# Kernel tuning notes

Hardware: AMD Instinct MI355X
Metric: run time of the kernel (lower is better)

Reference implementation:

```python
import jax, jax.numpy as jnp
import numpy as np

B, T, D, H, L, V = 8, 1024, 1024, 16, 4, 50257
HD = D // H
DF = 4 * D
EPS = 1e-5


def _layernorm(x, w, b):
    m = jnp.mean(x, axis=-1, keepdims=True)
    v = jnp.mean((x - m) ** 2, axis=-1, keepdims=True)
    return (x - m) * jax.lax.rsqrt(v + EPS) * w + b


def setup_inputs() -> dict:
    key = jax.random.key(0)
    ks = jax.random.split(key, 17)
    s = 0.02
    n = lambda k, shape: (jax.random.normal(k, shape) * s).astype(jnp.float32)
    return {
        "idx": jax.random.randint(ks[0], (B, T), 0, V),
        "tok_emb": n(ks[1], (V, D)),
        "pos_emb": n(ks[2], (T, D)),
        "wq": n(ks[3], (L, D, D)),
        "wk": n(ks[4], (L, D, D)),
        "wv": n(ks[5], (L, D, D)),
        "w_proj": n(ks[6], (L, D, D)),
        "b_proj": jnp.zeros((L, D), jnp.float32),
        "ln1_w": jnp.ones((L, D), jnp.float32),
        "ln1_b": jnp.zeros((L, D), jnp.float32),
        "ln2_w": jnp.ones((L, D), jnp.float32),
        "ln2_b": jnp.zeros((L, D), jnp.float32),
        "w1": n(ks[7], (L, D, DF)),
        "b1": jnp.zeros((L, DF), jnp.float32),
        "w2": n(ks[8], (L, DF, D)),
        "b2": jnp.zeros((L, D), jnp.float32),
    }


def reference(idx, tok_emb, pos_emb, wq, wk, wv, w_proj, b_proj,
              ln1_w, ln1_b, ln2_w, ln2_b, w1, b1, w2, b2):
    b, t = idx.shape
    x = tok_emb[idx] + pos_emb[:t]  # [B,T,D]
    causal_mask = jnp.tril(jnp.ones((t, t), dtype=bool))  # [T,T]
    # NOTE: original scales by full embedding dim C**-0.5, not head_size
    scale = jnp.asarray(D, x.dtype) ** -0.5
    for l in range(L):
        h = _layernorm(x, ln1_w[l], ln1_b[l])
        q = (h @ wq[l]).reshape(b, t, H, HD)
        k = (h @ wk[l]).reshape(b, t, H, HD)
        v = (h @ wv[l]).reshape(b, t, H, HD)
        scores = jnp.einsum('bthd,bshd->bhts', q, k) * scale  # [B,H,T,T]
        scores = jnp.where(causal_mask, scores, -jnp.inf)
        attn = jax.nn.softmax(scores, axis=-1)
        ctx = jnp.einsum('bhts,bshd->bthd', attn, v).reshape(b, t, D)
        x = x + (ctx @ w_proj[l] + b_proj[l])
        h2 = _layernorm(x, ln2_w[l], ln2_b[l])
        ff = jax.nn.relu(h2 @ w1[l] + b1[l]) @ w2[l] + b2[l]
        x = x + ff  # fRes = 1.0 (linear_residual=True)
    return x
```

## Files before the change

### kernel.cpp

```cpp
#include <hip/hip_runtime.h>
#include <hip/hip_bf16.h>
#include <stdint.h>

typedef __hip_bfloat16 bf16;
typedef __attribute__((ext_vector_type(8))) short short8;
typedef __attribute__((ext_vector_type(4))) float f32x4;
typedef __attribute__((ext_vector_type(2))) unsigned int uint32x2;

static constexpr int TB = 8;
static constexpr int TT = 1024;
static constexpr int TD = 1024;
static constexpr int TH = 16;
static constexpr int TL = 4;
static constexpr int TDF = 4096;
static constexpr int TM = TB * TT;
static constexpr int QS = 3072;

#if __has_builtin(__builtin_amdgcn_permlane16_swap) && __has_builtin(__builtin_amdgcn_permlane32_swap)
#define USE_PERMLANE 1
#else
#define USE_PERMLANE 0
#endif

#define GLOAD16(g, l) __builtin_amdgcn_global_load_lds( \
    (const __attribute__((address_space(1))) unsigned int*)(g), \
    (__attribute__((address_space(3))) unsigned int*)(l), 16, 0, 0)

__global__ __launch_bounds__(256) void k_embed(const int* __restrict__ idx,
        const float* __restrict__ tok, const float* __restrict__ pos,
        bf16* __restrict__ xbf) {
    int row = blockIdx.x;
    int t = row & (TT - 1);
    int token = idx[row];
    int c = threadIdx.x * 4;
    float4 tv = *(const float4*)(tok + (int64_t)token * TD + c);
    float4 pv = *(const float4*)(pos + (int64_t)t * TD + c);
    bf16 t4[4];
    t4[0] = __float2bfloat16(tv.x + pv.x);
    t4[1] = __float2bfloat16(tv.y + pv.y);
    t4[2] = __float2bfloat16(tv.z + pv.z);
    t4[3] = __float2bfloat16(tv.w + pv.w);
    *(uint2*)(xbf + (int64_t)row * TD + c) = *(uint2*)t4;
}

__global__ __launch_bounds__(256) void k_ln(const bf16* __restrict__ x,
        const float* __restrict__ w, const float* __restrict__ b,
        bf16* __restrict__ out) {
    int row = blockIdx.x;
    int tid = threadIdx.x;
    const bf16* xr = x + (int64_t)row * TD;
    uint2 raw = *(const uint2*)(xr + tid * 4);
    const bf16* rp = (const bf16*)&raw;
    float v0 = __bfloat162float(rp[0]), v1 = __bfloat162float(rp[1]);
    float v2 = __bfloat162float(rp[2]), v3 = __bfloat162float(rp[3]);
    float s  = v0 + v1 + v2 + v3;
    float s2 = v0*v0 + v1*v1 + v2*v2 + v3*v3;
    #pragma unroll
    for (int off = 32; off; off >>= 1) { s += __shfl_xor(s, off); s2 += __shfl_xor(s2, off); }
    __shared__ float red[8];
    int wv_ = tid >> 6, ln_ = tid & 63;
    if (ln_ == 0) { red[wv_] = s; red[4 + wv_] = s2; }
    __syncthreads();
    s  = red[0] + red[1] + red[2] + red[3];
    s2 = red[4] + red[5] + red[6] + red[7];
    float mean = s * (1.f / TD);
    float var  = s2 * (1.f / TD) - mean * mean;
    float rstd = rsqrtf(var + 1e-5f);
    float4 wv4 = *(const float4*)(w + tid * 4);
    float4 bv4 = *(const float4*)(b + tid * 4);
    bf16 t4[4];
    t4[0] = __float2bfloat16((v0 - mean) * rstd * wv4.x + bv4.x);
    t4[1] = __float2bfloat16((v1 - mean) * rstd * wv4.y + bv4.y);
    t4[2] = __float2bfloat16((v2 - mean) * rstd * wv4.z + bv4.z);
    t4[3] = __float2bfloat16((v3 - mean) * rstd * wv4.w + bv4.w);
    *(uint2*)(out + (int64_t)row * TD + tid * 4) = *(uint2*)t4;
}

__global__ __launch_bounds__(256) void k_wt(
        const float* __restrict__ wq, const float* __restrict__ wk,
        const float* __restrict__ wv, const float* __restrict__ wp,
        const float* __restrict__ w1, const float* __restrict__ w2,
        bf16* __restrict__ qkvT, bf16* __restrict__ wpT,
        bf16* __restrict__ w1T, bf16* __restrict__ w2T) {
    __shared__ bf16 tile[64 * 74];
    const int id = blockIdx.x;
    const float* src; bf16* dst; int K, N, n0, k0;
    if (id < 768) {
        int w = id >> 8, r = id & 255;
        src = (w == 0) ? wq : ((w == 1) ? wk : wv);
        dst = qkvT + (int64_t)w * 1024 * 1024;
        K = 1024; N = 1024; n0 = (r & 15) * 64; k0 = (r >> 4) * 64;
    } else if (id < 1024) {
        int r = id - 768; src = wp; dst = wpT;
        K = 1024; N = 1024; n0 = (r & 15) * 64; k0 = (r >> 4) * 64;
    } else if (id < 2048) {
        int r = id - 1024; src = w1; dst = w1T;
        K = 1024; N = 4096; n0 = (r & 63) * 64; k0 = (r >> 6) * 64;
    } else {
        int r = id - 2048; src = w2; dst = w2T;
        K = 4096; N = 1024; n0 = (r & 15) * 64; k0 = (r >> 4) * 64;
    }
    const int tid = threadIdx.x;
    #pragma unroll
    for (int i = 0; i < 16; i++) {
        int q = i * 256 + tid;
        int r = q >> 6, c = q & 63;
        tile[r * 74 + c] = __float2bfloat16(src[(int64_t)(k0 + r) * N + n0 + c]);
    }
    __syncthreads();
    #pragma unroll
    for (int i = 0; i < 16; i++) {
        int q = i * 256 + tid;
        int nr = q >> 6, kc = q & 63;
        dst[(int64_t)(n0 + nr) * K + k0 + kc] = tile[kc * 74 + nr];
    }
}

template<int EPI>
__global__ __launch_bounds__(512, 2) void k_gemm256(const bf16* __restrict__ A,
        const bf16* __restrict__ BT, const float* __restrict__ bias,
        float* __restrict__ outF, bf16* __restrict__ outB,
        bf16* __restrict__ vtp, int M, int N, int K) {
    extern __shared__ __align__(16) char smem[];
    const int tid = threadIdx.x;
    const int lane = tid & 63, wave = tid >> 6;
    const int wm = wave >> 2, wn = wave & 3;
    const int lr = lane & 15, lk = lane >> 4;
    const int nb = gridDim.x;
    const int sb = (blockIdx.x & 7) * (nb >> 3) + (blockIdx.x >> 3);
    const int nbn = N >> 8;
    const int bm = sb / nbn, bn = sb % nbn;
    const int64_t aBase = (int64_t)bm * 256 * K;
    const int64_t bBase = (int64_t)bn * 256 * K;
    const int NT = K >> 6;

    const int tswz = tid ^ (((tid >> 5) & 1) << 1);
    const int row0 = tswz >> 3, s0 = tswz & 7;

#define STAGE256(tt) do { \
        char* Ad_ = smem + (((tt) & 1) << 15); \
        char* Bd_ = smem + 65536 + (((tt) & 1) << 15); \
        _Pragma("unroll") \
        for (int j = 0; j < 4; j++) { \
            const int rr_ = j * 64 + row0; \
            GLOAD16(A  + aBase + (int64_t)rr_ * K + (tt) * 64 + s0 * 8, Ad_ + (j * 512 + tid) * 16); \
            GLOAD16(BT + bBase + (int64_t)rr_ * K + (tt) * 64 + s0 * 8, Bd_ + (j * 512 + tid) * 16); \
        } \
    } while (0)

    f32x4 acc[8][4] = {};
    const int lkx = lk ^ ((lr & 4) >> 1);
    const int aoff = wm * 8192 + lr * 64 + lkx * 8;
    const int boff = wn * 4096 + lr * 64 + lkx * 8;

    STAGE256(0);
    STAGE256(1);
    asm volatile("s_waitcnt vmcnt(8)" ::: "memory");
    __builtin_amdgcn_s_barrier();

    for (int t = 0; t < NT; ++t) {
        const bf16* Ab = (const bf16*)(smem + ((t & 1) << 15));
        const bf16* Bb = (const bf16*)(smem + 65536 + ((t & 1) << 15));
        short8 af[2][8], bv[2][4];
        #pragma unroll
        for (int kk = 0; kk < 2; kk++) {
            #pragma unroll
            for (int m = 0; m < 8; m++)
                af[kk][m] = *(const short8*)(Ab + aoff + m * 1024 + kk * 32);
            #pragma unroll
            for (int n = 0; n < 4; n++)
                bv[kk][n] = *(const short8*)(Bb + boff + n * 1024 + kk * 32);
        }
        asm volatile("s_waitcnt lgkmcnt(0)" ::: "memory");
        __builtin_amdgcn_sched_barrier(0);
        __builtin_amdgcn_s_barrier();
        if (t + 2 < NT) STAGE256(t + 2);
        __builtin_amdgcn_s_setprio(1);
        #pragma unroll
        for (int kk = 0; kk < 2; kk++)
            #pragma unroll
            for (int fm = 0; fm < 8; fm++)
                #pragma unroll
                for (int fn = 0; fn < 4; fn++)
                    acc[fm][fn] = __builtin_amdgcn_mfma_f32_16x16x32_bf16(
                        af[kk][fm], bv[kk][fn], acc[fm][fn], 0, 0, 0);
        __builtin_amdgcn_s_setprio(0);
        if (t + 2 < NT) {
            asm volatile("s_waitcnt vmcnt(8)" ::: "memory");
            __builtin_amdgcn_s_barrier();
        } else if (t + 1 < NT) {
            asm volatile("s_waitcnt vmcnt(0)" ::: "memory");
            __builtin_amdgcn_s_barrier();
        }
    }
#undef STAGE256

    #pragma unroll
    for (int fm = 0; fm < 8; fm++) {
        #pragma unroll
        for (int fn = 0; fn < 4; fn++) {
            const int col = bn * 256 + wn * 64 + fn * 16 + lr;
            if constexpr (EPI & 16) {
                const int trow = bm * 256 + wm * 128 + fm * 16 + lk * 4;
                if (col >= 2048) {
                    const int d = col - 2048;
                    bf16 t4[4];
                    #pragma unroll
                    for (int r = 0; r < 4; r++)
                        t4[r] = __float2bfloat16(acc[fm][fn][r]);
                    const int bb = trow >> 10, tt2 = trow & 1023;
                    *(uint2*)(vtp + ((int64_t)((bb * TH + (d >> 6)) * 64 + (d & 63)) * TT + tt2)) = *(uint2*)t4;
                } else {
                    #pragma unroll
                    for (int r = 0; r < 4; r++)
                        outB[(int64_t)(trow + r) * N + col] = __float2bfloat16(acc[fm][fn][r]);
                }
            } else {
                #pragma unroll
                for (int r = 0; r < 4; r++) {
                    const int row = bm * 256 + wm * 128 + fm * 16 + lk * 4 + r;
                    float v = acc[fm][fn][r];
                    if constexpr (EPI & 1) v += bias[col];
                    if constexpr (EPI & 2) v = fmaxf(v, 0.f);
                    if constexpr (EPI & 8) outF[(int64_t)row * N + col] = v;
                    else outB[(int64_t)row * N + col] = __float2bfloat16(v);
                }
            }
        }
    }
}

template<int EPI>
__global__ __launch_bounds__(512, 2) void k_gemm128d(const bf16* __restrict__ A,
        const bf16* __restrict__ BT, const float* __restrict__ bias,
        const bf16* __restrict__ residB,
        float* __restrict__ outF, bf16* __restrict__ outB, int M, int N, int K) {
    extern __shared__ __align__(16) char smem[];
    const int tid = threadIdx.x;
    const int lane = tid & 63, wave = tid >> 6;
    const int wm = wave >> 2, wn = wave & 3;
    const int lr = lane & 15, lk = lane >> 4;
    const int nb = gridDim.x;
    const int sb = (blockIdx.x & 7) * (nb >> 3) + (blockIdx.x >> 3);
    const int nbn = N >> 7;
    const int bm = sb / nbn, bn = sb % nbn;
    const int64_t aBase = (int64_t)bm * 128 * K;
    const int64_t bBase = (int64_t)bn * 128 * K;
    const int NT = K >> 6;

    const int tswz = tid ^ (((tid >> 5) & 1) << 1);
    const int row0 = tswz >> 3, s0 = tswz & 7;

#define STAGE128D(tt) do { \
        char* Ad_ = smem + (((tt) & 1) << 14); \
        char* Bd_ = smem + 32768 + (((tt) & 1) << 14); \
        _Pragma("unroll") \
        for (int j = 0; j < 2; j++) { \
            const int rr_ = j * 64 + row0; \
            GLOAD16(A  + aBase + (int64_t)rr_ * K + (tt) * 64 + s0 * 8, Ad_ + (j * 512 + tid) * 16); \
            GLOAD16(BT + bBase + (int64_t)rr_ * K + (tt) * 64 + s0 * 8, Bd_ + (j * 512 + tid) * 16); \
        } \
    } while (0)

    f32x4 acc[4][2] = {};
    const int lkx = lk ^ ((lr & 4) >> 1);
    const int aoff = wm * 4096 + lr * 64 + lkx * 8;
    const int boff = wn * 2048 + lr * 64 + lkx * 8;

    STAGE128D(0);
    STAGE128D(1);
    asm volatile("s_waitcnt vmcnt(4)" ::: "memory");
    __builtin_amdgcn_s_barrier();

    for (int t = 0; t < NT; ++t) {
        const bf16* Ab = (const bf16*)(smem + ((t & 1) << 14));
        const bf16* Bb = (const bf16*)(smem + 32768 + ((t & 1) << 14));
        short8 af[2][4], bv[2][2];
        #pragma unroll
        for (int kk = 0; kk < 2; kk++) {
            #pragma unroll
            for (int m = 0; m < 4; m++)
                af[kk][m] = *(const short8*)(Ab + aoff + m * 1024 + kk * 32);
            #pragma unroll
            for (int n = 0; n < 2; n++)
                bv[kk][n] = *(const short8*)(Bb + boff + n * 1024 + kk * 32);
        }
        asm volatile("s_waitcnt lgkmcnt(0)" ::: "memory");
        __builtin_amdgcn_sched_barrier(0);
        __builtin_amdgcn_s_barrier();
        if (t + 2 < NT) STAGE128D(t + 2);
        __builtin_amdgcn_s_setprio(1);
        #pragma unroll
        for (int kk = 0; kk < 2; kk++)
            #pragma unroll
            for (int fm = 0; fm < 4; fm++)
                #pragma unroll
                for (int fn = 0; fn < 2; fn++)
                    acc[fm][fn] = __builtin_amdgcn_mfma_f32_16x16x32_bf16(
                        af[kk][fm], bv[kk][fn], acc[fm][fn], 0, 0, 0);
        __builtin_amdgcn_s_setprio(0);
        if (t + 2 < NT) {
            asm volatile("s_waitcnt vmcnt(4)" ::: "memory");
            __builtin_amdgcn_s_barrier();
        } else if (t + 1 < NT) {
            asm volatile("s_waitcnt vmcnt(0)" ::: "memory");
            __builtin_amdgcn_s_barrier();
        }
    }
#undef STAGE128D

    #pragma unroll
    for (int fm = 0; fm < 4; fm++) {
        #pragma unroll
        for (int fn = 0; fn < 2; fn++) {
            const int col = bn * 128 + wn * 32 + fn * 16 + lr;
            #pragma unroll
            for (int r = 0; r < 4; r++) {
                const int row = bm * 128 + wm * 64 + fm * 16 + lk * 4 + r;
                float v = acc[fm][fn][r];
                if constexpr (EPI & 1) v += bias[col];
                if constexpr (EPI & 2) v = fmaxf(v, 0.f);
                if constexpr (EPI & 4) v += __bfloat162float(residB[(int64_t)row * N + col]);
                if constexpr (EPI & 8) outF[(int64_t)row * N + col] = v;
                else outB[(int64_t)row * N + col] = __float2bfloat16(v);
            }
        }
    }
}

#if USE_PERMLANE
__device__ __forceinline__ float redmax16(float v) {
    uint32x2 s = __builtin_amdgcn_permlane16_swap(
        __float_as_uint(v), __float_as_uint(v), false, false);
    return fmaxf(__uint_as_float(s[0]), __uint_as_float(s[1]));
}
__device__ __forceinline__ float redmax32(float v) {
    uint32x2 s = __builtin_amdgcn_permlane32_swap(
        __float_as_uint(v), __float_as_uint(v), false, false);
    return fmaxf(__uint_as_float(s[0]), __uint_as_float(s[1]));
}
#endif

__device__ __forceinline__ void attn_tile(int k0, int qg, int nk,
        short8 qf0, short8 qf1,
        short8 kf00, short8 kf01, short8 kf10, short8 kf11,
        const short8 (&vf)[4], f32x4 (&ctx)[4], float& mrun, float& lrun,
        int c, int g, float scale2) {
    f32x4 st0 = {}, st1 = {};
    __builtin_amdgcn_s_setprio(1);
    st0 = __builtin_amdgcn_mfma_f32_16x16x32_bf16(kf00, qf0, st0, 0, 0, 0);
    st0 = __builtin_amdgcn_mfma_f32_16x16x32_bf16(kf01, qf1, st0, 0, 0, 0);
    const bool h2 = (k0 + 16 < nk);
    if (h2) {
        st1 = __builtin_amdgcn_mfma_f32_16x16x32_bf16(kf10, qf0, st1, 0, 0, 0);
        st1 = __builtin_amdgcn_mfma_f32_16x16x32_bf16(kf11, qf1, st1, 0, 0, 0);
    }
    __builtin_amdgcn_s_setprio(0);
    float sv[8];
    #pragma unroll
    for (int r = 0; r < 4; r++) {
        int kg = k0 + 4 * g + r;
        sv[r] = (kg <= qg) ? st0[r] * scale2 : -INFINITY;
    }
    #pragma unroll
    for (int r = 0; r < 4; r++) {
        int kg = k0 + 16 + 4 * g + r;
        sv[4 + r] = (h2 && kg <= qg) ? st1[r] * scale2 : -INFINITY;
    }
    float bm = sv[0];
    #pragma unroll
    for (int i = 1; i < 8; i++) bm = fmaxf(bm, sv[i]);
#if USE_PERMLANE
    bm = redmax32(redmax16(bm));
#else
    bm = fmaxf(bm, __shfl_xor(bm, 16));
    bm = fmaxf(bm, __shfl_xor(bm, 32));
#endif
    if (__any(bm > mrun + 11.5416f)) {
        const float mnew = fmaxf(mrun, bm);
        const float facc = exp2f(mrun - mnew);
        lrun *= facc;
        #pragma unroll
        for (int dt = 0; dt < 4; dt++) ctx[dt] *= facc;
        mrun = mnew;
    }
    float p[8], psum = 0.f;
    #pragma unroll
    for (int i = 0; i < 8; i++) { p[i] = exp2f(sv[i] - mrun); psum += p[i]; }
    lrun += psum;

    auto pk = [](float a, float b2) -> uint32_t {
        uint16_t lo = __hip_bfloat16_raw(__float2bfloat16(a)).x;
        uint16_t hi = __hip_bfloat16_raw(__float2bfloat16(b2)).x;
        return (uint32_t)lo | ((uint32_t)hi << 16);
    };
    uint32_t w00 = pk(p[0], p[1]), w01 = pk(p[2], p[3]);
    uint32_t w10 = pk(p[4], p[5]), w11 = pk(p[6], p[7]);
    union { uint32_t u[4]; short8 v; } pa;
#if USE_PERMLANE
    uint32x2 sA = __builtin_amdgcn_permlane32_swap(w00, w10, false, false);
    uint32x2 sA2 = __builtin_amdgcn_permlane16_swap(sA[0], sA[1], false, false);
    uint32x2 sB = __builtin_amdgcn_permlane32_swap(w01, w11, false, false);
    uint32x2 sB2 = __builtin_amdgcn_permlane16_swap(sB[0], sB[1], false, false);
    pa.u[0] = sA2[0]; pa.u[2] = sA2[1];
    pa.u[1] = sB2[0]; pa.u[3] = sB2[1];
#else
    const int srcA = c + ((g & 1) << 5);
    const int srcB = srcA + 16;
    uint32_t x0 = (uint32_t)__shfl((int)w00, srcA);
    uint32_t x1 = (uint32_t)__shfl((int)w01, srcA);
    uint32_t x2 = (uint32_t)__shfl((int)w00, srcB);
    uint32_t x3 = (uint32_t)__shfl((int)w01, srcB);
    uint32_t y0 = (uint32_t)__shfl((int)w10, srcA);
    uint32_t y1 = (uint32_t)__shfl((int)w11, srcA);
    uint32_t y2 = (uint32_t)__shfl((int)w10, srcB);
    uint32_t y3 = (uint32_t)__shfl((int)w11, srcB);
    const bool hi2 = (g >= 2);
    pa.u[0] = hi2 ? y0 : x0; pa.u[1] = hi2 ? y1 : x1;
    pa.u[2] = hi2 ? y2 : x2; pa.u[3] = hi2 ? y3 : x3;
#endif

    __builtin_amdgcn_s_setprio(1);
    #pragma unroll
    for (int dt = 0; dt < 4; dt++)
        ctx[dt] = __builtin_amdgcn_mfma_f32_16x16x32_bf16(vf[dt], pa.v, ctx[dt], 0, 0, 0);
    __builtin_amdgcn_s_setprio(0);
}

__global__ __launch_bounds__(512) void k_attn6(const bf16* __restrict__ qkv,
        const bf16* __restrict__ Vt, bf16* __restrict__ O) {
    __shared__ __align__(16) bf16 kv[3][2][64 * 64];
    const int tid = threadIdx.x;
    const int lane = tid & 63;
    const int wave = tid >> 6;
    const int sbid = (blockIdx.x & 7) * 64 + (blockIdx.x >> 3);
    const int qp = ((sbid * 8) & 31) + wave;
    const int h = (sbid >> 2) & 15, b = sbid >> 6;
    const int q0A = qp * 16, q0B = (63 - qp) * 16;
    const int c = lane & 15, g = lane >> 4;
    const int qgA = q0A + c, qgB = q0B + c;
    const float scale2 = 1.4426950408889634f / 32.0f;

    const bf16* Qp = qkv;
    const bf16* qrowA = Qp + ((int64_t)(b * TT + q0A + c)) * QS + h * 64 + g * 8;
    short8 qA0 = *(const short8*)(qrowA);
    short8 qA1 = *(const short8*)(qrowA + 32);
    const bf16* qrowB = Qp + ((int64_t)(b * TT + q0B + c)) * QS + h * 64 + g * 8;
    short8 qB0 = *(const short8*)(qrowB);
    short8 qB1 = *(const short8*)(qrowB + 32);

    f32x4 ctxA[4] = {}, ctxB[4] = {};
    float mA = -INFINITY, lA = 0.f, mB = -INFINITY, lB = 0.f;

    const bf16* kg = qkv + 1024 + ((int64_t)b * TT) * QS + h * 64;
    const bf16* vg = Vt + ((int64_t)(b * TH + h) * 64) * TT;

    const int nkA = q0A + 16, nkB = q0B + 16;
    const int nkMax = (63 - ((sbid * 8) & 31)) * 16 + 16;

    const int row0 = tid >> 3, s0 = tid & 7, sx = (s0 ^ (row0 & 7)) * 8;

#define STAGEKV(bi, K0) do { \
        GLOAD16(kg + (int64_t)((K0) + row0) * QS + sx, &kv[bi][0][tid * 8]); \
        GLOAD16(vg + (int64_t)row0 * TT + (K0) + sx,   &kv[bi][1][tid * 8]); \
    } while (0)

    auto kread = [&](int bi, int row, int ch) -> short8 {
        return *(const short8*)&kv[bi][0][row * 64 + ((ch ^ (row & 7)) * 8)];
    };
    auto vread = [&](int bi, int row, int ch) -> short8 {
        return *(const short8*)&kv[bi][1][row * 64 + ((ch ^ (row & 7)) * 8)];
    };

    STAGEKV(0, 0);
    if (64 < nkMax) STAGEKV(1, 64);

    int bi = 0;
    for (int k0 = 0; k0 < nkMax; k0 += 64) {
        if (k0 + 64 < nkMax)
            asm volatile("s_waitcnt vmcnt(2)" ::: "memory");
        else
            asm volatile("s_waitcnt vmcnt(0)" ::: "memory");
        __syncthreads();
        const int bn2 = (bi + 2 >= 3) ? bi - 1 : bi + 2;
        if (k0 + 128 < nkMax) STAGEKV(bn2, k0 + 128);
        #pragma unroll
        for (int sb2 = 0; sb2 < 2; sb2++) {
            const int kl = sb2 * 32;
            const int ks = k0 + kl;
            if (ks < nkB) {
                short8 kf00 = kread(bi, kl + c, g);
                short8 kf01 = kread(bi, kl + c, g + 4);
                short8 kf10 = kread(bi, kl + 16 + c, g);
                short8 kf11 = kread(bi, kl + 16 + c, g + 4);
                short8 vf[4];
                #pragma unroll
                for (int dt = 0; dt < 4; dt++)
                    vf[dt] = vread(bi, dt * 16 + c, (sb2 << 2) + g);
                attn_tile(ks, qgB, nkB, qB0, qB1, kf00, kf01, kf10, kf11, vf,
                          ctxB, mB, lB, c, g, scale2);
                if (ks < nkA)
                    attn_tile(ks, qgA, nkA, qA0, qA1, kf00, kf01, kf10, kf11, vf,
                              ctxA, mA, lA, c, g, scale2);
            }
        }
        bi = (bi + 1 == 3) ? 0 : bi + 1;
    }
#undef STAGEKV

    lA += __shfl_xor(lA, 16); lA += __shfl_xor(lA, 32);
    lB += __shfl_xor(lB, 16); lB += __shfl_xor(lB, 32);

    const float invA = 1.0f / lA, invB = 1.0f / lB;
    bf16* orowA = O + ((int64_t)(b * TT + q0A + c)) * TD + h * 64 + g * 4;
    bf16* orowB = O + ((int64_t)(b * TT + q0B + c)) * TD + h * 64 + g * 4;
    #pragma unroll
    for (int dt = 0; dt < 4; dt++) {
        bf16 t4[4];
        #pragma unroll
        for (int r = 0; r < 4; r++) t4[r] = __float2bfloat16(ctxA[dt][r] * invA);
        *(uint2*)(orowA + dt * 16) = *(uint2*)t4;
        #pragma unroll
        for (int r = 0; r < 4; r++) t4[r] = __float2bfloat16(ctxB[dt][r] * invB);
        *(uint2*)(orowB + dt * 16) = *(uint2*)t4;
    }
}

extern "C" void kernel_launch(void* const* d_in, const int* in_sizes, int n_in,
                              void* d_out, int out_size, void* d_ws, size_t ws_size,
                              hipStream_t stream) {
    const int*   idx  = (const int*)  d_in[0];
    const float* tok  = (const float*)d_in[1];
    const float* pos  = (const float*)d_in[2];
    const float* wq   = (const float*)d_in[3];
    const float* wk   = (const float*)d_in[4];
    const float* wv   = (const float*)d_in[5];
    const float* wp   = (const float*)d_in[6];
    const float* bp   = (const float*)d_in[7];
    const float* ln1w = (const float*)d_in[8];
    const float* ln1b = (const float*)d_in[9];
    const float* ln2w = (const float*)d_in[10];
    const float* ln2b = (const float*)d_in[11];
    const float* w1   = (const float*)d_in[12];
    const float* b1   = (const float*)d_in[13];
    const float* w2   = (const float*)d_in[14];
    const float* b2   = (const float*)d_in[15];
    float* xout = (float*)d_out;

    char* ws = (char*)d_ws;
    size_t off = 0;
    auto alloc = [&](size_t bytes) {
        char* p = ws + off; off += (bytes + 255) & ~(size_t)255; return p;
    };
    bf16* xbf  = (bf16*)alloc((size_t)TM * TD * 2);
    bf16* h    = (bf16*)alloc((size_t)TM * TD * 2);
    bf16* qkv  = (bf16*)alloc((size_t)TM * QS * 2);
    bf16* ctx  = (bf16*)alloc((size_t)TM * TD * 2);
    bf16* ffa  = (bf16*)alloc((size_t)TM * TDF * 2);
    bf16* qkvT = (bf16*)alloc((size_t)3 * TD * TD * 2);
    bf16* wpT  = (bf16*)alloc((size_t)TD * TD * 2);
    bf16* w1T  = (bf16*)alloc((size_t)TD * TDF * 2);
    bf16* w2T  = (bf16*)alloc((size_t)TD * TDF * 2);
    bf16* vt   = (bf16*)ffa;

    hipFuncSetAttribute((const void*)k_gemm256<16>,
        hipFuncAttributeMaxDynamicSharedMemorySize, 131072);
    hipFuncSetAttribute((const void*)k_gemm256<3>,
        hipFuncAttributeMaxDynamicSharedMemorySize, 131072);
    hipFuncSetAttribute((const void*)k_gemm128d<5>,
        hipFuncAttributeMaxDynamicSharedMemorySize, 65536);
    hipFuncSetAttribute((const void*)k_gemm128d<13>,
        hipFuncAttributeMaxDynamicSharedMemorySize, 65536);

    k_embed<<<TM, 256, 0, stream>>>(idx, tok, pos, xbf);

    const int gQKV = (TM / 256) * (QS / 256);
    const int gF1  = (TM / 256) * (TDF / 256);
    const int gN1K = (TM / 128) * (TD / 128);

    for (int l = 0; l < TL; l++) {
        k_wt<<<3072, 256, 0, stream>>>(
            wq + (int64_t)l * TD * TD, wk + (int64_t)l * TD * TD,
            wv + (int64_t)l * TD * TD, wp + (int64_t)l * TD * TD,
            w1 + (int64_t)l * TD * TDF, w2 + (int64_t)l * TDF * TD,
            qkvT, wpT, w1T, w2T);

        k_ln<<<TM, 256, 0, stream>>>(xbf, ln1w + l * TD, ln1b + l * TD, h);
        k_gemm256<16><<<gQKV, 512, 131072, stream>>>(h, qkvT, nullptr, nullptr, qkv, vt, TM, QS, TD);
        k_attn6<<<512, 512, 0, stream>>>(qkv, vt, ctx);
        k_gemm128d<5><<<gN1K, 512, 65536, stream>>>(ctx, wpT, bp + l * TD, xbf, nullptr, xbf, TM, TD, TD);
        k_ln<<<TM, 256, 0, stream>>>(xbf, ln2w + l * TD, ln2b + l * TD, h);
        k_gemm256<3><<<gF1, 512, 131072, stream>>>(h, w1T, b1 + l * TDF, nullptr, ffa, nullptr, TM, TDF, TD);
        if (l + 1 < TL)
            k_gemm128d<5><<<gN1K, 512, 65536, stream>>>(ffa, w2T, b2 + l * TD, xbf, nullptr, xbf, TM, TD, TDF);
        else
            k_gemm128d<13><<<gN1K, 512, 65536, stream>>>(ffa, w2T, b2 + l * TD, xbf, xout, nullptr, TM, TD, TDF);
    }
    (void)in_sizes; (void)n_in; (void)out_size; (void)ws_size;
}
```

Before: 1.322 ms.

## Batch weight transposes across layers, fuse embed with LN1, one row per wave in LN

```diff
diff --git a/kernel.cpp b/kernel.cpp
--- a/kernel.cpp
+++ b/kernel.cpp
@@ -26,63 +26,103 @@
     (const __attribute__((address_space(1))) unsigned int*)(g), \
     (__attribute__((address_space(3))) unsigned int*)(l), 16, 0, 0)
 
-__global__ __launch_bounds__(256) void k_embed(const int* __restrict__ idx,
+__global__ __launch_bounds__(256) void k_embed_ln(const int* __restrict__ idx,
         const float* __restrict__ tok, const float* __restrict__ pos,
-        bf16* __restrict__ xbf) {
-    int row = blockIdx.x;
-    int t = row & (TT - 1);
-    int token = idx[row];
-    int c = threadIdx.x * 4;
-    float4 tv = *(const float4*)(tok + (int64_t)token * TD + c);
-    float4 pv = *(const float4*)(pos + (int64_t)t * TD + c);
-    bf16 t4[4];
-    t4[0] = __float2bfloat16(tv.x + pv.x);
-    t4[1] = __float2bfloat16(tv.y + pv.y);
-    t4[2] = __float2bfloat16(tv.z + pv.z);
-    t4[3] = __float2bfloat16(tv.w + pv.w);
-    *(uint2*)(xbf + (int64_t)row * TD + c) = *(uint2*)t4;
+        const float* __restrict__ w, const float* __restrict__ b,
+        bf16* __restrict__ xbf, bf16* __restrict__ h) {
+    const int wv = threadIdx.x >> 6, lane = threadIdx.x & 63;
+    const int row = blockIdx.x * 4 + wv;
+    const int t = row & (TT - 1);
+    const int token = idx[row];
+    float v[16];
+    float s = 0.f, s2 = 0.f;
+    #pragma unroll
+    for (int i = 0; i < 4; i++) {
+        const int c = i * 256 + lane * 4;
+        float4 tv = *(const float4*)(tok + (int64_t)token * TD + c);
+        float4 pv = *(const float4*)(pos + (int64_t)t * TD + c);
+        v[i*4+0] = tv.x + pv.x; v[i*4+1] = tv.y + pv.y;
+        v[i*4+2] = tv.z + pv.z; v[i*4+3] = tv.w + pv.w;
+        bf16 t4[4];
+        #pragma unroll
+        for (int j = 0; j < 4; j++) t4[j] = __float2bfloat16(v[i*4+j]);
+        *(uint2*)(xbf + (int64_t)row * TD + c) = *(uint2*)t4;
+        #pragma unroll
+        for (int j = 0; j < 4; j++) { s += v[i*4+j]; s2 += v[i*4+j]*v[i*4+j]; }
+    }
+    #pragma unroll
+    for (int off = 32; off; off >>= 1) { s += __shfl_xor(s, off); s2 += __shfl_xor(s2, off); }
+    const float mean = s * (1.f / TD);
+    const float rstd = rsqrtf(s2 * (1.f / TD) - mean * mean + 1e-5f);
+    #pragma unroll
+    for (int i = 0; i < 4; i++) {
+        const int c = i * 256 + lane * 4;
+        float4 wv4 = *(const float4*)(w + c);
+        float4 bv4 = *(const float4*)(b + c);
+        bf16 t4[4];
+        t4[0] = __float2bfloat16((v[i*4+0] - mean) * rstd * wv4.x + bv4.x);
+        t4[1] = __float2bfloat16((v[i*4+1] - mean) * rstd * wv4.y + bv4.y);
+        t4[2] = __float2bfloat16((v[i*4+2] - mean) * rstd * wv4.z + bv4.z);
+        t4[3] = __float2bfloat16((v[i*4+3] - mean) * rstd * wv4.w + bv4.w);
+        *(uint2*)(h + (int64_t)row * TD + c) = *(uint2*)t4;
+    }
 }
 
 __global__ __launch_bounds__(256) void k_ln(const bf16* __restrict__ x,
         const float* __restrict__ w, const float* __restrict__ b,
         bf16* __restrict__ out) {
-    int row = blockIdx.x;
-    int tid = threadIdx.x;
+    const int wv = threadIdx.x >> 6, lane = threadIdx.x & 63;
+    const int row = blockIdx.x * 4 + wv;
     const bf16* xr = x + (int64_t)row * TD;
-    uint2 raw = *(const uint2*)(xr + tid * 4);
-    const bf16* rp = (const bf16*)&raw;
-    float v0 = __bfloat162float(rp[0]), v1 = __bfloat162float(rp[1]);
-    float v2 = __bfloat162float(rp[2]), v3 = __bfloat162float(rp[3]);
-    float s  = v0 + v1 + v2 + v3;
-    float s2 = v0*v0 + v1*v1 + v2*v2 + v3*v3;
+    float v[16];
+    float s = 0.f, s2 = 0.f;
+    #pragma unroll
+    for (int i = 0; i < 4; i++) {
+        const int c = i * 256 + lane * 4;
+        uint2 raw = *(const uint2*)(xr + c);
+        const bf16* rp = (const bf16*)&raw;
+        #pragma unroll
+        for (int j = 0; j < 4; j++) {
+            v[i*4+j] = __bfloat162float(rp[j]);
+            s += v[i*4+j]; s2 += v[i*4+j]*v[i*4+j];
+        }
+    }
     #pragma unroll
     for (int off = 32; off; off >>= 1) { s += __shfl_xor(s, off); s2 += __shfl_xor(s2, off); }
-    __shared__ float red[8];
-    int wv_ = tid >> 6, ln_ = tid & 63;
-    if (ln_ == 0) { red[wv_] = s; red[4 + wv_] = s2; }
-    __syncthreads();
-    s  = red[0] + red[1] + red[2] + red[3];
-    s2 = red[4] + red[5] + red[6] + red[7];
-    float mean = s * (1.f / TD);
-    float var  = s2 * (1.f / TD) - mean * mean;
-    float rstd = rsqrtf(var + 1e-5f);
-    float4 wv4 = *(const float4*)(w + tid * 4);
-    float4 bv4 = *(const float4*)(b + tid * 4);
-    bf16 t4[4];
-    t4[0] = __float2bfloat16((v0 - mean) * rstd * wv4.x + bv4.x);
-    t4[1] = __float2bfloat16((v1 - mean) * rstd * wv4.y + bv4.y);
-    t4[2] = __float2bfloat16((v2 - mean) * rstd * wv4.z + bv4.z);
-    t4[3] = __float2bfloat16((v3 - mean) * rstd * wv4.w + bv4.w);
-    *(uint2*)(out + (int64_t)row * TD + tid * 4) = *(uint2*)t4;
+    const float mean = s * (1.f / TD);
+    const float rstd = rsqrtf(s2 * (1.f / TD) - mean * mean + 1e-5f);
+    #pragma unroll
+    for (int i = 0; i < 4; i++) {
+        const int c = i * 256 + lane * 4;
+        float4 wv4 = *(const float4*)(w + c);
+        float4 bv4 = *(const float4*)(b + c);
+        bf16 t4[4];
+        t4[0] = __float2bfloat16((v[i*4+0] - mean) * rstd * wv4.x + bv4.x);
+        t4[1] = __float2bfloat16((v[i*4+1] - mean) * rstd * wv4.y + bv4.y);
+        t4[2] = __float2bfloat16((v[i*4+2] - mean) * rstd * wv4.z + bv4.z);
+        t4[3] = __float2bfloat16((v[i*4+3] - mean) * rstd * wv4.w + bv4.w);
+        *(uint2*)(out + (int64_t)row * TD + c) = *(uint2*)t4;
+    }
 }
 
 __global__ __launch_bounds__(256) void k_wt(
-        const float* __restrict__ wq, const float* __restrict__ wk,
-        const float* __restrict__ wv, const float* __restrict__ wp,
-        const float* __restrict__ w1, const float* __restrict__ w2,
-        bf16* __restrict__ qkvT, bf16* __restrict__ wpT,
-        bf16* __restrict__ w1T, bf16* __restrict__ w2T) {
+        const float* __restrict__ wq0, const float* __restrict__ wk0,
+        const float* __restrict__ wv0, const float* __restrict__ wp0,
+        const float* __restrict__ w10, const float* __restrict__ w20,
+        bf16* __restrict__ qkvT0, bf16* __restrict__ wpT0,
+        bf16* __restrict__ w1T0, bf16* __restrict__ w2T0) {
     __shared__ bf16 tile[64 * 74];
+    const int l = blockIdx.y;
+    const float* wq = wq0 + (int64_t)l * TD * TD;
+    const float* wk = wk0 + (int64_t)l * TD * TD;
+    const float* wv = wv0 + (int64_t)l * TD * TD;
+    const float* wp = wp0 + (int64_t)l * TD * TD;
+    const float* w1 = w10 + (int64_t)l * TD * TDF;
+    const float* w2 = w20 + (int64_t)l * TDF * TD;
+    bf16* qkvT = qkvT0 + (int64_t)l * 3 * TD * TD;
+    bf16* wpT  = wpT0  + (int64_t)l * TD * TD;
+    bf16* w1T  = w1T0  + (int64_t)l * TD * TDF;
+    bf16* w2T  = w2T0  + (int64_t)l * TDF * TD;
     const int id = blockIdx.x;
     const float* src; bf16* dst; int K, N, n0, k0;
     if (id < 768) {
@@ -557,10 +597,10 @@
     bf16* qkv  = (bf16*)alloc((size_t)TM * QS * 2);
     bf16* ctx  = (bf16*)alloc((size_t)TM * TD * 2);
     bf16* ffa  = (bf16*)alloc((size_t)TM * TDF * 2);
-    bf16* qkvT = (bf16*)alloc((size_t)3 * TD * TD * 2);
-    bf16* wpT  = (bf16*)alloc((size_t)TD * TD * 2);
-    bf16* w1T  = (bf16*)alloc((size_t)TD * TDF * 2);
-    bf16* w2T  = (bf16*)alloc((size_t)TD * TDF * 2);
+    bf16* qkvT = (bf16*)alloc((size_t)TL * 3 * TD * TD * 2);
+    bf16* wpT  = (bf16*)alloc((size_t)TL * TD * TD * 2);
+    bf16* w1T  = (bf16*)alloc((size_t)TL * TD * TDF * 2);
+    bf16* w2T  = (bf16*)alloc((size_t)TL * TD * TDF * 2);
     bf16* vt   = (bf16*)ffa;
 
     hipFuncSetAttribute((const void*)k_gemm256<16>,
@@ -572,29 +612,31 @@
     hipFuncSetAttribute((const void*)k_gemm128d<13>,
         hipFuncAttributeMaxDynamicSharedMemorySize, 65536);
 
-    k_embed<<<TM, 256, 0, stream>>>(idx, tok, pos, xbf);
+    k_wt<<<dim3(3072, TL), 256, 0, stream>>>(wq, wk, wv, wp, w1, w2,
+                                             qkvT, wpT, w1T, w2T);
+    k_embed_ln<<<TM / 4, 256, 0, stream>>>(idx, tok, pos, ln1w, ln1b, xbf, h);
 
     const int gQKV = (TM / 256) * (QS / 256);
     const int gF1  = (TM / 256) * (TDF / 256);
     const int gN1K = (TM / 128) * (TD / 128);
 
     for (int l = 0; l < TL; l++) {
-        k_wt<<<3072, 256, 0, stream>>>(
-            wq + (int64_t)l * TD * TD, wk + (int64_t)l * TD * TD,
-            wv + (int64_t)l * TD * TD, wp + (int64_t)l * TD * TD,
-            w1 + (int64_t)l * TD * TDF, w2 + (int64_t)l * TDF * TD,
-            qkvT, wpT, w1T, w2T);
-
-        k_ln<<<TM, 256, 0, stream>>>(xbf, ln1w + l * TD, ln1b + l * TD, h);
-        k_gemm256<16><<<gQKV, 512, 131072, stream>>>(h, qkvT, nullptr, nullptr, qkv, vt, TM, QS, TD);
+        const bf16* qkvTl = qkvT + (int64_t)l * 3 * TD * TD;
+        const bf16* wpTl  = wpT  + (int64_t)l * TD * TD;
+        const bf16* w1Tl  = w1T  + (int64_t)l * TD * TDF;
+        const bf16* w2Tl  = w2T  + (int64_t)l * TDF * TD;
+
+        if (l > 0)
+            k_ln<<<TM / 4, 256, 0, stream>>>(xbf, ln1w + l * TD, ln1b + l * TD, h);
+        k_gemm256<16><<<gQKV, 512, 131072, stream>>>(h, qkvTl, nullptr, nullptr, qkv, vt, TM, QS, TD);
         k_attn6<<<512, 512, 0, stream>>>(qkv, vt, ctx);
-        k_gemm128d<5><<<gN1K, 512, 65536, stream>>>(ctx, wpT, bp + l * TD, xbf, nullptr, xbf, TM, TD, TD);
-        k_ln<<<TM, 256, 0, stream>>>(xbf, ln2w + l * TD, ln2b + l * TD, h);
-        k_gemm256<3><<<gF1, 512, 131072, stream>>>(h, w1T, b1 + l * TDF, nullptr, ffa, nullptr, TM, TDF, TD);
+        k_gemm128d<5><<<gN1K, 512, 65536, stream>>>(ctx, wpTl, bp + l * TD, xbf, nullptr, xbf, TM, TD, TD);
+        k_ln<<<TM / 4, 256, 0, stream>>>(xbf, ln2w + l * TD, ln2b + l * TD, h);
+        k_gemm256<3><<<gF1, 512, 131072, stream>>>(h, w1Tl, b1 + l * TDF, nullptr, ffa, nullptr, TM, TDF, TD);
         if (l + 1 < TL)
-            k_gemm128d<5><<<gN1K, 512, 65536, stream>>>(ffa, w2T, b2 + l * TD, xbf, nullptr, xbf, TM, TD, TDF);
+            k_gemm128d<5><<<gN1K, 512, 65536, stream>>>(ffa, w2Tl, b2 + l * TD, xbf, nullptr, xbf, TM, TD, TDF);
         else
-            k_gemm128d<13><<<gN1K, 512, 65536, stream>>>(ffa, w2T, b2 + l * TD, xbf, xout, nullptr, TM, TD, TDF);
+            k_gemm128d<13><<<gN1K, 512, 65536, stream>>>(ffa, w2Tl, b2 + l * TD, xbf, xout, nullptr, TM, TD, TDF);
     }
     (void)in_sizes; (void)n_in; (void)out_size; (void)ws_size;
 }
```

New measurement: 1.375 ms. 1.04x slower.
